# Kernel optimization log

Hardware: AMD Instinct MI355X
Metric: run time of the kernel (lower is better)

## Reference

```python
import jax, jax.numpy as jnp
import numpy as np

H = 256
W = 256
RADIUS = 1.5
TAU = 1.0
EPS = 1e-8


def _ndc_grid(h, w):
    ys, xs = jnp.meshgrid(jnp.arange(h, dtype=jnp.float32), jnp.arange(w, dtype=jnp.float32), indexing='ij')
    xs = xs / (w - 1) * 2.0 - 1.0
    ys = ys / (h - 1) * 2.0 - 1.0
    return jnp.stack([xs.ravel(), ys.ravel()], 0)  # [2, N]


def _make_rt(key, b, v):
    # near-identity extrinsics: identity rotation + small random translation
    t = jax.random.normal(key, (b, v, 3), dtype=jnp.float32) * 0.05
    rt = jnp.tile(jnp.eye(4, dtype=jnp.float32), (b, v, 1, 1))
    rt = rt.at[:, :, :3, 3].set(t)
    return rt


def setup_inputs() -> dict:
    key = jax.random.key(0)
    ks = jax.random.split(key, 4)
    B, V, C = 2, 3, 32
    depths = jax.random.uniform(ks[0], (B, V, 1, H, W), jnp.float32, 1.0, 3.0)
    feats = jax.random.normal(ks[1], (B, V, C, H, W), jnp.float32)
    K = jnp.tile(jnp.eye(4, dtype=jnp.float32), (B, 1, 1))
    K = K.at[:, 0, 0].set(1.2).at[:, 1, 1].set(1.2)  # NDC-space focal lengths
    src_RTs = _make_rt(ks[2], B, V)
    src_RTinvs = jnp.linalg.inv(src_RTs)
    dst_RTs = _make_rt(ks[3], B, 1)
    dst_RTinvs = jnp.linalg.inv(dst_RTs)
    return {"depths": depths, "feats": feats, "K": K, "src_RTs": src_RTs,
            "src_RTinvs": src_RTinvs, "dst_RTs": dst_RTs, "dst_RTinvs": dst_RTinvs}


def _view_to_world(depth, K_inv, RTinv):
    # depth: [BV, 1, N] -> world homogeneous coords [BV, 4, N]
    grid = _ndc_grid(H, W)                                      # [2, N]
    xy = grid[None] * depth                                     # [BV, 2, N]
    pc = jnp.concatenate([xy, depth, jnp.ones_like(depth)], 1)  # [BV, 4, N]
    cam = jnp.einsum('bij,bjn->bin', K_inv, pc)
    return jnp.einsum('bij,bjn->bin', RTinv, cam)


def _world_to_view(wrld, K, RT):
    cam = jnp.einsum('bij,bjn->bin', RT, wrld)
    proj = jnp.einsum('bij,bjn->bin', K, cam)
    z = proj[:, 2:3]
    xy = proj[:, 0:2] / (z + EPS)
    xy = jnp.where(z <= 0.0, -10.0, xy)       # invalid points pushed off-screen
    return jnp.concatenate([xy, z], 1)        # [BV, 3, N]


def _splatter(pc, feats, radius):
    # pc: [BV, N, 3] (x_ndc, y_ndc, depth); feats: [BV, C, N]
    BV, N, _ = pc.shape
    C = feats.shape[1]
    x, y, z = pc[..., 0], pc[..., 1], pc[..., 2]
    px = (x + 1.0) * 0.5 * (W - 1)
    py = (y + 1.0) * 0.5 * (H - 1)
    offs = jnp.array([[dy, dx] for dy in (-1, 0, 1) for dx in (-1, 0, 1)], dtype=jnp.float32)
    ix = jnp.round(px)[..., None] + offs[:, 1]     # [BV, N, 9]
    iy = jnp.round(py)[..., None] + offs[:, 0]
    dist = jnp.sqrt((ix - px[..., None]) ** 2 + (iy - py[..., None]) ** 2 + EPS)
    w_r = jnp.maximum(0.0, 1.0 - dist / radius)    # radius-based falloff
    valid = (ix >= 0) & (ix < W) & (iy >= 0) & (iy < H) & (z[..., None] > 0)
    w_d = jnp.exp(-TAU * z)[..., None]             # depth-aware (soft z-buffer) weight
    w = w_r * w_d * valid.astype(w_r.dtype)        # [BV, N, 9]
    idx = iy.astype(jnp.int32).clip(0, H - 1) * W + ix.astype(jnp.int32).clip(0, W - 1)
    flat = (jnp.arange(BV, dtype=jnp.int32)[:, None, None] * (H * W) + idx).reshape(-1)
    w_sum = jax.ops.segment_sum(w.reshape(-1), flat, num_segments=BV * H * W)
    fw = (feats[:, :, :, None] * w[:, None, :, :]).transpose(0, 2, 3, 1).reshape(-1, C)
    f_sum = jax.ops.segment_sum(fw, flat, num_segments=BV * H * W)
    z_sum = jax.ops.segment_sum((z[..., None] * w).reshape(-1), flat, num_segments=BV * H * W)
    out_f = (f_sum / (w_sum[:, None] + EPS)).reshape(BV, H, W, C).transpose(0, 3, 1, 2)
    out_d = (z_sum / (w_sum + EPS)).reshape(BV, 1, H, W)
    return out_f, out_d


def reference(depths, feats, K, src_RTs, src_RTinvs, dst_RTs, dst_RTinvs):
    B, V, C = feats.shape[0], feats.shape[1], feats.shape[2]
    N = H * W
    d = depths.reshape(B * V, 1, N)
    f = feats.reshape(B * V, C, N)
    K_bv = jnp.repeat(K, V, axis=0)
    K_inv_bv = jnp.repeat(jnp.linalg.inv(K), V, axis=0)
    src_rtinv = src_RTinvs.reshape(B * V, 4, 4)
    dst_rt = jnp.repeat(dst_RTs[:, 0], V, axis=0)
    wrld = _view_to_world(d, K_inv_bv, src_rtinv)      # view -> world per source view
    sampler = _world_to_view(wrld, K_bv, dst_rt)       # world -> target view [BV,3,N]
    pc = sampler.transpose(0, 2, 1)                    # [BV, N, 3]
    prj_f, prj_d = _splatter(pc, f, RADIUS)
    return prj_f.reshape(B, V, C, H, W), prj_d.reshape(B, V, 1, H, W)
```

## Files before the change

kernel.cpp:

```cpp
#include <hip/hip_runtime.h>
#include <hip/hip_fp16.h>
#include <math.h>

#define H 256
#define W 256
#define HW (H * W)
#define B 2
#define V 3
#define BV (B * V)
#define C 32
#define RADIUS 1.5f
#define TAU 1.0f
#define EPS 1e-8f

#define NPIX (BV * HW)
#define NBLK (NPIX / 256)

#define GW 258
#define GH 258
#define NCELL (BV * GH * GW)
#define NALLOC_BLK ((NCELL + 255) / 256)

__device__ __forceinline__ int swizzle_block(int bid) {
    return (bid & 7) * (NBLK / 8) + (bid >> 3);
}

__global__ void setup_kernel(const float* __restrict__ Kmat,
                             const float* __restrict__ srcRTinv,
                             const float* __restrict__ dstRT,
                             float* __restrict__ Mbuf) {
    int bv = threadIdx.x;
    if (bv >= BV) return;
    int b = bv / V;

    float a[4][8];
    for (int i = 0; i < 4; i++)
        for (int j = 0; j < 4; j++) {
            a[i][j] = Kmat[b * 16 + i * 4 + j];
            a[i][4 + j] = (i == j) ? 1.0f : 0.0f;
        }
    for (int col = 0; col < 4; col++) {
        int piv = col;
        float best = fabsf(a[col][col]);
        for (int r = col + 1; r < 4; r++) {
            float v = fabsf(a[r][col]);
            if (v > best) { best = v; piv = r; }
        }
        if (piv != col) {
            for (int j = 0; j < 8; j++) {
                float t = a[col][j]; a[col][j] = a[piv][j]; a[piv][j] = t;
            }
        }
        float s = 1.0f / a[col][col];
        for (int j = 0; j < 8; j++) a[col][j] *= s;
        for (int r = 0; r < 4; r++) {
            if (r == col) continue;
            float m = a[r][col];
            for (int j = 0; j < 8; j++) a[r][j] -= m * a[col][j];
        }
    }
    float Kinv[16];
    for (int i = 0; i < 4; i++)
        for (int j = 0; j < 4; j++) Kinv[i * 4 + j] = a[i][4 + j];

    float T1[16];
    const float* S = srcRTinv + bv * 16;
    for (int i = 0; i < 4; i++)
        for (int j = 0; j < 4; j++) {
            float acc = 0.0f;
            for (int k = 0; k < 4; k++) acc += S[i * 4 + k] * Kinv[k * 4 + j];
            T1[i * 4 + j] = acc;
        }
    float T2[16];
    const float* D = dstRT + b * 16;
    for (int i = 0; i < 4; i++)
        for (int j = 0; j < 4; j++) {
            float acc = 0.0f;
            for (int k = 0; k < 4; k++) acc += D[i * 4 + k] * T1[k * 4 + j];
            T2[i * 4 + j] = acc;
        }
    const float* Kb = Kmat + b * 16;
    for (int i = 0; i < 4; i++)
        for (int j = 0; j < 4; j++) {
            float acc = 0.0f;
            for (int k = 0; k < 4; k++) acc += Kb[i * 4 + k] * T2[k * 4 + j];
            Mbuf[bv * 16 + i * 4 + j] = acc;
        }
}

__global__ __launch_bounds__(256) void project_count_kernel(
    const float* __restrict__ depths, const float* __restrict__ Mbuf,
    float4* __restrict__ staging, int2* __restrict__ meta) {
    int gid = swizzle_block(blockIdx.x) * 256 + threadIdx.x;
    int bv = gid >> 16;
    int n = gid & (HW - 1);

    float xn = (float)(n & (W - 1)) * (2.0f / (W - 1)) - 1.0f;
    float yn = (float)(n >> 8)      * (2.0f / (H - 1)) - 1.0f;
    float d = depths[gid];
    const float* M = Mbuf + bv * 16;
    float X = xn * d, Y = yn * d;
    float p0 = M[0] * X + M[1] * Y + M[2] * d + M[3];
    float p1 = M[4] * X + M[5] * Y + M[6] * d + M[7];
    float z  = M[8] * X + M[9] * Y + M[10] * d + M[11];

    int cell = -1;
    float px = 0.0f, py = 0.0f;
    if (z > 0.0f) {
        float inv = 1.0f / (z + EPS);
        px = (p0 * inv + 1.0f) * 0.5f * (float)(W - 1);
        py = (p1 * inv + 1.0f) * 0.5f * (float)(H - 1);
        float rx = rintf(px), ry = rintf(py);
        if (rx >= -1.0f && rx <= (float)W && ry >= -1.0f && ry <= (float)H) {
            cell = bv * (GH * GW) + ((int)ry + 1) * GW + ((int)rx + 1);
            atomicAdd(&meta[cell].y, 1);
        }
    }
    staging[gid] = make_float4(px, py, z, __int_as_float(cell));
}

__global__ __launch_bounds__(256) void alloc_kernel(int2* __restrict__ meta,
                                                    int* __restrict__ total) {
    int i = blockIdx.x * 256 + threadIdx.x;
    int c = (i < NCELL) ? meta[i].y : 0;
    int lane = threadIdx.x & 63;
    int wid = threadIdx.x >> 6;
    int x = c;
#pragma unroll
    for (int dlt = 1; dlt < 64; dlt <<= 1) {
        int y = __shfl_up(x, dlt);
        if (lane >= dlt) x += y;
    }
    __shared__ int wsum[4];
    __shared__ int wbase[4];
    __shared__ int bbase;
    if (lane == 63) wsum[wid] = x;
    __syncthreads();
    if (threadIdx.x == 0) {
        int s0 = wsum[0], s1 = wsum[1], s2 = wsum[2], s3 = wsum[3];
        wbase[0] = 0; wbase[1] = s0; wbase[2] = s0 + s1; wbase[3] = s0 + s1 + s2;
        bbase = atomicAdd(total, s0 + s1 + s2 + s3);
    }
    __syncthreads();
    if (i < NCELL) meta[i].x = bbase + wbase[wid] + (x - c);
}

__global__ __launch_bounds__(256) void fill_kernel(
    const float* __restrict__ feats, const float4* __restrict__ staging,
    int2* __restrict__ meta, float4* __restrict__ entries16,
    uint4* __restrict__ entriesF) {
    __shared__ float sm[C][257];
    int blk = blockIdx.x;
    int bv = blk >> 8;
    int n0 = (blk & 255) << 8;
    int tid = threadIdx.x;
    const float* src = feats + (size_t)bv * C * HW + n0;
#pragma unroll
    for (int c = 0; c < C; c++) sm[c][tid] = src[(size_t)c * HW + tid];
    __syncthreads();

    int gid = (bv << 16) | (n0 + tid);
    float4 s = staging[gid];
    int cell = __float_as_int(s.w);
    if (cell < 0) return;
    int pos = atomicAdd(&meta[cell].x, 1);

    float wd = expf(-TAU * s.z);
    entries16[pos] = make_float4(s.x, s.y, s.z, wd);

    uint4* dst = entriesF + (size_t)pos * 4;
#pragma unroll
    for (int g = 0; g < 4; g++) {
        __half2 h0 = __floats2half2_rn(sm[g * 8 + 0][tid], sm[g * 8 + 1][tid]);
        __half2 h1 = __floats2half2_rn(sm[g * 8 + 2][tid], sm[g * 8 + 3][tid]);
        __half2 h2 = __floats2half2_rn(sm[g * 8 + 4][tid], sm[g * 8 + 5][tid]);
        __half2 h3 = __floats2half2_rn(sm[g * 8 + 6][tid], sm[g * 8 + 7][tid]);
        uint4 pk;
        pk.x = *(unsigned int*)&h0;
        pk.y = *(unsigned int*)&h1;
        pk.z = *(unsigned int*)&h2;
        pk.w = *(unsigned int*)&h3;
        dst[g] = pk;
    }
}

__global__ __launch_bounds__(256) void gather_kernel(
    const float4* __restrict__ entries16, const uint4* __restrict__ entriesF,
    const int2* __restrict__ meta, float* __restrict__ out) {
    int gid = swizzle_block(blockIdx.x) * 256 + threadIdx.x;
    int bv = gid >> 16;
    int q = gid & (HW - 1);
    float qx = (float)(q & (W - 1));
    float qy = (float)(q >> 8);

    float wsum = 0.0f, zwsum = 0.0f;
    float facc[C];
#pragma unroll
    for (int c = 0; c < C; c++) facc[c] = 0.0f;

    int cbase = bv * (GH * GW);
#pragma unroll
    for (int dy = 0; dy < 3; dy++) {
        int rowbase = cbase + ((q >> 8) + dy) * GW + (q & (W - 1));
#pragma unroll
        for (int dx = 0; dx < 3; dx++) {
            int2 m2 = meta[rowbase + dx];
            int cnt = m2.y;
            int pos0 = m2.x - cnt;
            for (int j = 0; j < cnt; j++) {
                float4 v = entries16[pos0 + j];
                float ddx = qx - v.x, ddy = qy - v.y;
                float d2 = ddx * ddx + ddy * ddy + EPS;
                if (d2 < RADIUS * RADIUS) {
                    float dist = sqrtf(d2);
                    float wr = fmaxf(0.0f, 1.0f - dist * (1.0f / RADIUS));
                    float w = wr * v.w;
                    wsum += w;
                    zwsum += v.z * w;
                    const uint4* fp = entriesF + (size_t)(pos0 + j) * 4;
#pragma unroll
                    for (int g = 0; g < 4; g++) {
                        uint4 fv = fp[g];
                        const __half2* h2 = (const __half2*)&fv;
#pragma unroll
                        for (int k = 0; k < 4; k++) {
                            float2 f2 = __half22float2(h2[k]);
                            facc[g * 8 + 2 * k]     = fmaf(w, f2.x, facc[g * 8 + 2 * k]);
                            facc[g * 8 + 2 * k + 1] = fmaf(w, f2.y, facc[g * 8 + 2 * k + 1]);
                        }
                    }
                }
            }
        }
    }

    float invw = 1.0f / (wsum + EPS);
    float* ob = out + (size_t)bv * C * HW + q;
#pragma unroll
    for (int c = 0; c < C; c++) ob[(size_t)c * HW] = facc[c] * invw;
    out[(size_t)BV * C * HW + gid] = zwsum * invw;
}

extern "C" void kernel_launch(void* const* d_in, const int* in_sizes, int n_in,
                              void* d_out, int out_size, void* d_ws, size_t ws_size,
                              hipStream_t stream) {
    const float* depths   = (const float*)d_in[0];
    const float* feats    = (const float*)d_in[1];
    const float* Kmat     = (const float*)d_in[2];
    const float* srcRTinv = (const float*)d_in[4];
    const float* dstRT    = (const float*)d_in[5];
    float* out = (float*)d_out;

    char* ws = (char*)d_ws;
    size_t off_entriesF = 0;
    size_t off_entries16 = off_entriesF + (size_t)NPIX * 64;
    size_t off_staging = off_entries16 + (size_t)NPIX * 16;
    size_t off_meta = off_staging + (size_t)NPIX * 16;
    size_t off_total = off_meta + (size_t)NCELL * 8;
    size_t off_M = off_total + 16;
    size_t needed = off_M + (size_t)BV * 16 * 4;

    if (ws_size < needed) {
        hipMemsetAsync(d_out, 0, (size_t)out_size * 4, stream);
        return;
    }

    uint4* entriesF   = (uint4*)(ws + off_entriesF);
    float4* entries16 = (float4*)(ws + off_entries16);
    float4* staging   = (float4*)(ws + off_staging);
    int2* meta        = (int2*)(ws + off_meta);
    int* total        = (int*)(ws + off_total);
    float* Mbuf       = (float*)(ws + off_M);

    hipMemsetAsync(meta, 0, (size_t)NCELL * 8 + 16, stream);
    setup_kernel<<<1, 64, 0, stream>>>(Kmat, srcRTinv, dstRT, Mbuf);
    project_count_kernel<<<NBLK, 256, 0, stream>>>(depths, Mbuf, staging, meta);
    alloc_kernel<<<NALLOC_BLK, 256, 0, stream>>>(meta, total);
    fill_kernel<<<NBLK, 256, 0, stream>>>(feats, staging, meta, entries16,
                                          entriesF);
    gather_kernel<<<NBLK, 256, 0, stream>>>(entries16, entriesF, meta, out);
}
```

Before: 220.7 us.

## Use ordered scan for cell offsets and 16x16 tiled gather with LDS staging

Replaces the atomic-order block allocation with a two-pass deterministic prefix scan (per-block local scan plus a single-block scan of block sums), so cell storage ends up in row-major order and a row of neighbouring cells is contiguous. The gather kernel now works on 16x16 pixel tiles: it loads cell start offsets for the 18x19 halo into LDS and stages up to 64 point entries per halo row in LDS. Each pixel then walks contiguous ranges of three cells per row instead of nine separate cells. This aims to cut scattered global reads of point metadata, at the cost of an extra serial single-block scan launch, more LDS and a spill path to global memory for long rows.

```diff
diff --git a/kernel.cpp b/kernel.cpp
--- a/kernel.cpp
+++ b/kernel.cpp
@@ -19,7 +19,8 @@
 #define GW 258
 #define GH 258
 #define NCELL (BV * GH * GW)
-#define NALLOC_BLK ((NCELL + 255) / 256)
+#define NSUMS ((NCELL + 255) / 256)
+#define ROWCAP 64
 
 __device__ __forceinline__ int swizzle_block(int bid) {
     return (bid & 7) * (NBLK / 8) + (bid >> 3);
@@ -119,8 +120,8 @@
     staging[gid] = make_float4(px, py, z, __int_as_float(cell));
 }
 
-__global__ __launch_bounds__(256) void alloc_kernel(int2* __restrict__ meta,
-                                                    int* __restrict__ total) {
+__global__ __launch_bounds__(256) void alloc1_kernel(int2* __restrict__ meta,
+                                                     int* __restrict__ bsum) {
     int i = blockIdx.x * 256 + threadIdx.x;
     int c = (i < NCELL) ? meta[i].y : 0;
     int lane = threadIdx.x & 63;
@@ -133,22 +134,55 @@
     }
     __shared__ int wsum[4];
     __shared__ int wbase[4];
-    __shared__ int bbase;
     if (lane == 63) wsum[wid] = x;
     __syncthreads();
     if (threadIdx.x == 0) {
         int s0 = wsum[0], s1 = wsum[1], s2 = wsum[2], s3 = wsum[3];
         wbase[0] = 0; wbase[1] = s0; wbase[2] = s0 + s1; wbase[3] = s0 + s1 + s2;
-        bbase = atomicAdd(total, s0 + s1 + s2 + s3);
-    }
-    __syncthreads();
-    if (i < NCELL) meta[i].x = bbase + wbase[wid] + (x - c);
+        bsum[blockIdx.x] = s0 + s1 + s2 + s3;
+    }
+    __syncthreads();
+    if (i <= NCELL) meta[i].x = wbase[wid] + (x - c);
+}
+
+__global__ __launch_bounds__(256) void alloc2_kernel(int* __restrict__ bsum) {
+    __shared__ int wsum[4];
+    __shared__ int wbase[4];
+    __shared__ int carry_s;
+    int tid = threadIdx.x;
+    int lane = tid & 63;
+    int wid = tid >> 6;
+    if (tid == 0) carry_s = 0;
+    __syncthreads();
+    const int nchunk = (NSUMS + 255) / 256;
+    for (int ch = 0; ch < nchunk; ch++) {
+        int i = ch * 256 + tid;
+        int c = (i < NSUMS) ? bsum[i] : 0;
+        int x = c;
+#pragma unroll
+        for (int dlt = 1; dlt < 64; dlt <<= 1) {
+            int y = __shfl_up(x, dlt);
+            if (lane >= dlt) x += y;
+        }
+        if (lane == 63) wsum[wid] = x;
+        __syncthreads();
+        if (tid == 0) {
+            int cr = carry_s;
+            int s0 = wsum[0], s1 = wsum[1], s2 = wsum[2], s3 = wsum[3];
+            wbase[0] = cr; wbase[1] = cr + s0; wbase[2] = cr + s0 + s1;
+            wbase[3] = cr + s0 + s1 + s2;
+            carry_s = cr + s0 + s1 + s2 + s3;
+        }
+        __syncthreads();
+        if (i < NSUMS) bsum[i] = wbase[wid] + (x - c);
+        __syncthreads();
+    }
 }
 
 __global__ __launch_bounds__(256) void fill_kernel(
     const float* __restrict__ feats, const float4* __restrict__ staging,
-    int2* __restrict__ meta, float4* __restrict__ entries16,
-    uint4* __restrict__ entriesF) {
+    const int* __restrict__ bsum, int2* __restrict__ meta,
+    float4* __restrict__ entries16, uint4* __restrict__ entriesF) {
     __shared__ float sm[C][257];
     int blk = blockIdx.x;
     int bv = blk >> 8;
@@ -163,7 +197,7 @@
     float4 s = staging[gid];
     int cell = __float_as_int(s.w);
     if (cell < 0) return;
-    int pos = atomicAdd(&meta[cell].x, 1);
+    int pos = bsum[cell >> 8] + atomicAdd(&meta[cell].x, 1);
 
     float wd = expf(-TAU * s.z);
     entries16[pos] = make_float4(s.x, s.y, s.z, wd);
@@ -186,54 +220,91 @@
 
 __global__ __launch_bounds__(256) void gather_kernel(
     const float4* __restrict__ entries16, const uint4* __restrict__ entriesF,
-    const int2* __restrict__ meta, float* __restrict__ out) {
-    int gid = swizzle_block(blockIdx.x) * 256 + threadIdx.x;
-    int bv = gid >> 16;
-    int q = gid & (HW - 1);
-    float qx = (float)(q & (W - 1));
-    float qy = (float)(q >> 8);
+    const int2* __restrict__ meta, const int* __restrict__ bsum,
+    float* __restrict__ out) {
+    __shared__ float4 lds_e[18][ROWCAP];
+    __shared__ int cs_s[18][19];
+    __shared__ int row_rs[18];
+    __shared__ int row_stg[18];
+
+    int sblk = swizzle_block(blockIdx.x);
+    int bv = sblk >> 8;
+    int t = sblk & 255;
+    int ty0 = (t >> 4) << 4;
+    int tx0 = (t & 15) << 4;
+    int tid = threadIdx.x;
+    int cellbase = bv * (GH * GW);
+
+    for (int i = tid; i < 18 * 19; i += 256) {
+        int hr = i / 19, lc = i - hr * 19;
+        int cg = cellbase + (ty0 + hr) * GW + (tx0 + lc);
+        int2 m = meta[cg];
+        cs_s[hr][lc] = bsum[cg >> 8] + m.x - m.y;
+    }
+    __syncthreads();
+    if (tid < 18) {
+        int rs = cs_s[tid][0];
+        row_rs[tid] = rs;
+        row_stg[tid] = min(cs_s[tid][18] - rs, ROWCAP);
+    }
+    __syncthreads();
+    {
+        int wid = tid >> 6, lane = tid & 63;
+        for (int hr = wid; hr < 18; hr += 4)
+            if (lane < row_stg[hr])
+                lds_e[hr][lane] = entries16[row_rs[hr] + lane];
+    }
+    __syncthreads();
+
+    int lx = tid & 15, ly = tid >> 4;
+    float qx = (float)(tx0 + lx);
+    float qy = (float)(ty0 + ly);
 
     float wsum = 0.0f, zwsum = 0.0f;
     float facc[C];
 #pragma unroll
     for (int c = 0; c < C; c++) facc[c] = 0.0f;
 
-    int cbase = bv * (GH * GW);
-#pragma unroll
-    for (int dy = 0; dy < 3; dy++) {
-        int rowbase = cbase + ((q >> 8) + dy) * GW + (q & (W - 1));
-#pragma unroll
-        for (int dx = 0; dx < 3; dx++) {
-            int2 m2 = meta[rowbase + dx];
-            int cnt = m2.y;
-            int pos0 = m2.x - cnt;
-            for (int j = 0; j < cnt; j++) {
-                float4 v = entries16[pos0 + j];
-                float ddx = qx - v.x, ddy = qy - v.y;
-                float d2 = ddx * ddx + ddy * ddy + EPS;
-                if (d2 < RADIUS * RADIUS) {
-                    float dist = sqrtf(d2);
-                    float wr = fmaxf(0.0f, 1.0f - dist * (1.0f / RADIUS));
-                    float w = wr * v.w;
-                    wsum += w;
-                    zwsum += v.z * w;
-                    const uint4* fp = entriesF + (size_t)(pos0 + j) * 4;
-#pragma unroll
-                    for (int g = 0; g < 4; g++) {
-                        uint4 fv = fp[g];
-                        const __half2* h2 = (const __half2*)&fv;
-#pragma unroll
-                        for (int k = 0; k < 4; k++) {
-                            float2 f2 = __half22float2(h2[k]);
-                            facc[g * 8 + 2 * k]     = fmaf(w, f2.x, facc[g * 8 + 2 * k]);
-                            facc[g * 8 + 2 * k + 1] = fmaf(w, f2.y, facc[g * 8 + 2 * k + 1]);
-                        }
-                    }
+    auto accum = [&](float4 v, int pos) {
+        float ddx = qx - v.x, ddy = qy - v.y;
+        float d2 = ddx * ddx + ddy * ddy + EPS;
+        if (d2 < RADIUS * RADIUS) {
+            float dist = sqrtf(d2);
+            float wr = 1.0f - dist * (1.0f / RADIUS);
+            float w = wr * v.w;
+            wsum += w;
+            zwsum += v.z * w;
+            const uint4* fp = entriesF + (size_t)pos * 4;
+#pragma unroll
+            for (int g = 0; g < 4; g++) {
+                uint4 fv = fp[g];
+                const __half2* h2 = (const __half2*)&fv;
+#pragma unroll
+                for (int k = 0; k < 4; k++) {
+                    float2 f2 = __half22float2(h2[k]);
+                    facc[g * 8 + 2 * k]     = fmaf(w, f2.x, facc[g * 8 + 2 * k]);
+                    facc[g * 8 + 2 * k + 1] = fmaf(w, f2.y, facc[g * 8 + 2 * k + 1]);
                 }
             }
         }
-    }
-
+    };
+
+#pragma unroll
+    for (int dy = 0; dy < 3; dy++) {
+        int hr = ly + dy;
+        int s = cs_s[hr][lx];
+        int e = cs_s[hr][lx + 3];
+        int rs = row_rs[hr];
+        int se = rs + row_stg[hr];
+        int e1 = min(e, se);
+        for (int pos = s; pos < e1; ++pos)
+            accum(lds_e[hr][pos - rs], pos);
+        for (int pos = max(s, se); pos < e; ++pos)
+            accum(entries16[pos], pos);
+    }
+
+    int q = ((ty0 + ly) << 8) | (tx0 + lx);
+    int gid = (bv << 16) | q;
     float invw = 1.0f / (wsum + EPS);
     float* ob = out + (size_t)bv * C * HW + q;
 #pragma unroll
@@ -256,8 +327,8 @@
     size_t off_entries16 = off_entriesF + (size_t)NPIX * 64;
     size_t off_staging = off_entries16 + (size_t)NPIX * 16;
     size_t off_meta = off_staging + (size_t)NPIX * 16;
-    size_t off_total = off_meta + (size_t)NCELL * 8;
-    size_t off_M = off_total + 16;
+    size_t off_bsum = off_meta + (size_t)(NCELL + 1) * 8;
+    size_t off_M = off_bsum + (size_t)NSUMS * 4 + 16;
     size_t needed = off_M + (size_t)BV * 16 * 4;
 
     if (ws_size < needed) {
@@ -269,14 +340,16 @@
     float4* entries16 = (float4*)(ws + off_entries16);
     float4* staging   = (float4*)(ws + off_staging);
     int2* meta        = (int2*)(ws + off_meta);
-    int* total        = (int*)(ws + off_total);
+    int* bsum         = (int*)(ws + off_bsum);
     float* Mbuf       = (float*)(ws + off_M);
 
-    hipMemsetAsync(meta, 0, (size_t)NCELL * 8 + 16, stream);
+    hipMemsetAsync(meta, 0, (size_t)(NCELL + 1) * 8, stream);
     setup_kernel<<<1, 64, 0, stream>>>(Kmat, srcRTinv, dstRT, Mbuf);
     project_count_kernel<<<NBLK, 256, 0, stream>>>(depths, Mbuf, staging, meta);
-    alloc_kernel<<<NALLOC_BLK, 256, 0, stream>>>(meta, total);
-    fill_kernel<<<NBLK, 256, 0, stream>>>(feats, staging, meta, entries16,
-                                          entriesF);
-    gather_kernel<<<NBLK, 256, 0, stream>>>(entries16, entriesF, meta, out);
-}
+    alloc1_kernel<<<NSUMS, 256, 0, stream>>>(meta, bsum);
+    alloc2_kernel<<<1, 256, 0, stream>>>(bsum);
+    fill_kernel<<<NBLK, 256, 0, stream>>>(feats, staging, bsum, meta,
+                                          entries16, entriesF);
+    gather_kernel<<<NBLK, 256, 0, stream>>>(entries16, entriesF, meta, bsum,
+                                            out);
+}
```

Result: faster. 183.9 us (-16.7%).
